# Optimization experiments

Measured on AMD Instinct MI355X. Metric: run time of the kernel, lower is better.

Reference implementation:

```python
import math
import jax, jax.numpy as jnp
import numpy as np

B, S, D = 16, 2048, 256

def setup_inputs() -> dict:
    key = jax.random.key(0)
    kq, kk, kv, km = jax.random.split(key, 4)
    q = jax.random.normal(kq, (B, S, D), dtype=jnp.float32)
    k = jax.random.normal(kk, (B, S, D), dtype=jnp.float32)
    v = jax.random.normal(kv, (B, S, D), dtype=jnp.float32)
    mask = jax.random.randint(km, (B, S, S), 0, 2, dtype=jnp.int32)
    return {"q": q, "k": k, "v": v, "mask": mask}

def reference(q, k, v, mask):
    dim_input = q.shape[-1]
    # scores: [B, S, S]
    scores = jnp.einsum('bqd,bkd->bqk', q, k) / math.sqrt(dim_input)
    # non-standard masking: masked positions set to 0.0 (NOT -inf) before softmax
    scores = jnp.where(mask == 0, jnp.float32(0.0), scores)
    att = jax.nn.softmax(scores, axis=-1)
    # original: if mask.sum() == 0, attention is all zeros
    att = jnp.where(mask.sum() > 0, att, jnp.zeros_like(att))
    return jnp.einsum('bqk,bkd->bqd', att, v)
```

## Files before the change

kernel.cpp:

```cpp
#include <hip/hip_runtime.h>


#define B_  16
#define S_  2048
#define D_  256
#define NT_ 64
#define TILE_BYTES 16384

typedef short bf16x8 __attribute__((ext_vector_type(8)));
typedef float f32x4  __attribute__((ext_vector_type(4)));

__device__ __forceinline__ unsigned short f2bf(float x) {
    union { float f; unsigned u; } c; c.f = x;
    unsigned u = c.u;
    u += 0x7FFFu + ((u >> 16) & 1u);
    return (unsigned short)(u >> 16);
}

#define GLDS(g, l) __builtin_amdgcn_global_load_lds( \
    (const __attribute__((address_space(1))) void*)(g), \
    (__attribute__((address_space(3))) void*)(l), 16, 0, 0)

#define WAITVM(N) asm volatile("s_waitcnt vmcnt(" #N ")" ::: "memory")

__global__ __launch_bounds__(256)
void prep_all(const float* __restrict__ k, const float* __restrict__ v,
              char* __restrict__ kbf, char* __restrict__ vtbf)
{
    const int bid = blockIdx.x;
    if (bid < 4096) {
        const int gid = bid * 256 + threadIdx.x;
        const int d8  = gid & 31;
        const int kv  = (gid >> 5) & 2047;
        const int b   = gid >> 16;
        const float* src = k + (((size_t)(b * S_ + kv)) << 8) + d8 * 8;
        const float4 f0 = *(const float4*)src;
        const float4 f1 = *(const float4*)(src + 4);
        bf16x8 h;
        h[0] = (short)f2bf(f0.x); h[1] = (short)f2bf(f0.y);
        h[2] = (short)f2bf(f0.z); h[3] = (short)f2bf(f0.w);
        h[4] = (short)f2bf(f1.x); h[5] = (short)f2bf(f1.y);
        h[6] = (short)f2bf(f1.z); h[7] = (short)f2bf(f1.w);
        const int tile = kv >> 5, kvl = kv & 31;
        char* dst = kbf + (((size_t)(b * NT_ + tile)) << 14)
                        + (kvl << 9) + ((d8 * 16) ^ ((kvl & 7) << 4));
        *(bf16x8*)dst = h;
    } else {
        const int gid  = (bid - 4096) * 256 + threadIdx.x;
        const int d    = gid & 255;
        const int g    = (gid >> 8) & 3;
        const int tile = (gid >> 10) & 63;
        const int b    = gid >> 16;
        const int kv0  = tile * 32 + g * 8;
        const float* src = v + (((size_t)(b * S_ + kv0)) << 8) + d;
        bf16x8 h;
        #pragma unroll
        for (int j = 0; j < 8; ++j) h[j] = (short)f2bf(src[(size_t)j << 8]);
        char* dst = vtbf + (((size_t)(b * NT_ + tile)) << 14)
                         + (d << 6) + ((g * 16) ^ (((d >> 1) & 3) << 4));
        *(bf16x8*)dst = h;
    }
}

__global__ __launch_bounds__(256, 1)
void attn_main(const float* __restrict__ q, const int* __restrict__ mask,
               const char* __restrict__ kbf, const char* __restrict__ vtbf,
               float* __restrict__ out)
{
    __shared__ alignas(128) char lds[139264];

    const int tid  = threadIdx.x;
    const int wid  = tid >> 6;
    const int lane = tid & 63;
    const int ln15 = lane & 15;
    const int quad = lane >> 4;
    const int swzK = (ln15 & 7) << 4;
    const int swzA = ((ln15 >> 1) & 3) << 4;

    const int bid = blockIdx.x;
    const int bx  = (bid & 7) * 32 + (bid >> 3);
    const int b   = bx >> 4;
    const int qt  = bx & 15;
    const int qw  = qt * 128 + wid * 32;

    const float QS = 0.09016844f;
    bf16x8 aq[2][8];
    #pragma unroll
    for (int s = 0; s < 2; ++s) {
        const float* qrow = q + ((size_t)(b * S_ + qw + s * 16 + ln15)) * D_;
        #pragma unroll
        for (int ks = 0; ks < 8; ++ks) {
            const float4 f0 = *(const float4*)(qrow + ks * 32 + quad * 8);
            const float4 f1 = *(const float4*)(qrow + ks * 32 + quad * 8 + 4);
            bf16x8 a;
            a[0] = (short)f2bf(f0.x * QS); a[1] = (short)f2bf(f0.y * QS);
            a[2] = (short)f2bf(f0.z * QS); a[3] = (short)f2bf(f0.w * QS);
            a[4] = (short)f2bf(f1.x * QS); a[5] = (short)f2bf(f1.y * QS);
            a[6] = (short)f2bf(f1.z * QS); a[7] = (short)f2bf(f1.w * QS);
            aq[s][ks] = a;
        }
    }
    __builtin_amdgcn_sched_barrier(0);

    bf16x8 ones;
    #pragma unroll
    for (int e = 0; e < 8; ++e) ones[e] = (short)0x3F80;

    f32x4 oacc[2][16];
    #pragma unroll
    for (int s = 0; s < 2; ++s)
        #pragma unroll
        for (int i = 0; i < 16; ++i) oacc[s][i] = (f32x4){0.f, 0.f, 0.f, 0.f};
    f32x4 lacc[2];
    lacc[0] = (f32x4){0.f, 0.f, 0.f, 0.f};
    lacc[1] = (f32x4){0.f, 0.f, 0.f, 0.f};

    const char* ktile = kbf  + (((size_t)b * NT_) << 14);
    const char* vtile = vtbf + (((size_t)b * NT_) << 14);
    char* pw = lds + 131072 + wid * 2048;
    const int cc = wid * 4;

    const int* mbase = mask + ((size_t)(b * S_ + qw + 4 * quad)) * S_;
    int mreg[4][16];

    #pragma unroll
    for (int t = 0; t < 3; ++t) {
        #pragma unroll
        for (int c = 0; c < 4; ++c) {
            GLDS(ktile + t * 16384 + (cc + c) * 1024 + lane * 16,
                 lds +         t * 16384 + (cc + c) * 1024);
            GLDS(vtile + t * 16384 + (cc + c) * 1024 + lane * 16,
                 lds + 65536 + t * 16384 + (cc + c) * 1024);
        }
        #pragma unroll
        for (int s = 0; s < 2; ++s)
            #pragma unroll
            for (int nt = 0; nt < 2; ++nt)
                #pragma unroll
                for (int r = 0; r < 4; ++r)
                    mreg[t][s * 8 + nt * 4 + r] = __builtin_nontemporal_load(
                        mbase + (size_t)(s * 16 + r) * S_ + t * 32 + nt * 16 + ln15);
    }

#define PHASE(T, CUR, CNT, ISSUE)                                               \
    {                                                                           \
        WAITVM(CNT);                                                            \
        __builtin_amdgcn_sched_barrier(0);                                      \
        __builtin_amdgcn_s_barrier();                                           \
        __builtin_amdgcn_sched_barrier(0);                                      \
        if (ISSUE) {                                                            \
            const int tn  = (T) + 3;                                            \
            const int bn  = ((CUR) + 3) & 3;                                    \
            const char* kg_ = ktile + ((size_t)tn << 14);                       \
            const char* vg_ = vtile + ((size_t)tn << 14);                       \
            _Pragma("unroll")                                                   \
            for (int c = 0; c < 4; ++c) {                                       \
                GLDS(kg_ + (cc + c) * 1024 + lane * 16,                         \
                     lds + bn * 16384 +         (cc + c) * 1024);               \
                GLDS(vg_ + (cc + c) * 1024 + lane * 16,                         \
                     lds + 65536 + bn * 16384 + (cc + c) * 1024);               \
            }                                                                   \
            _Pragma("unroll")                                                   \
            for (int s = 0; s < 2; ++s)                                         \
                _Pragma("unroll")                                               \
                for (int nt = 0; nt < 2; ++nt)                                  \
                    _Pragma("unroll")                                           \
                    for (int r = 0; r < 4; ++r)                                 \
                        mreg[bn][s * 8 + nt * 4 + r] = __builtin_nontemporal_load( \
                            mbase + (size_t)(s * 16 + r) * S_ + tn * 32 + nt * 16 + ln15); \
            __builtin_amdgcn_sched_barrier(0);                                  \
        }                                                                       \
        const char* kl = lds + (CUR) * 16384;                                   \
        f32x4 sacc[2][2];                                                       \
        sacc[0][0] = (f32x4){0.f, 0.f, 0.f, 0.f};                               \
        sacc[0][1] = (f32x4){0.f, 0.f, 0.f, 0.f};                               \
        sacc[1][0] = (f32x4){0.f, 0.f, 0.f, 0.f};                               \
        sacc[1][1] = (f32x4){0.f, 0.f, 0.f, 0.f};                               \
        _Pragma("unroll")                                                       \
        for (int ks = 0; ks < 8; ++ks) {                                        \
            _Pragma("unroll")                                                   \
            for (int nt = 0; nt < 2; ++nt) {                                    \
                const int off = ((nt * 16 + ln15) << 9)                         \
                              + (((ks << 6) + (quad << 4)) ^ swzK);             \
                const bf16x8 bk = *(const bf16x8*)(kl + off);                   \
                sacc[0][nt] = __builtin_amdgcn_mfma_f32_16x16x32_bf16(aq[0][ks], bk, sacc[0][nt], 0, 0, 0); \
                sacc[1][nt] = __builtin_amdgcn_mfma_f32_16x16x32_bf16(aq[1][ks], bk, sacc[1][nt], 0, 0, 0); \
            }                                                                   \
        }                                                                       \
        _Pragma("unroll")                                                       \
        for (int s = 0; s < 2; ++s) {                                           \
            _Pragma("unroll")                                                   \
            for (int nt = 0; nt < 2; ++nt) {                                    \
                _Pragma("unroll")                                               \
                for (int r = 0; r < 4; ++r) {                                   \
                    const float p = (mreg[CUR][s * 8 + nt * 4 + r] != 0)        \
                                  ? exp2f(sacc[s][nt][r]) : 1.0f;               \
                    const int row  = s * 16 + 4 * quad + r;                     \
                    const int boff = (row << 6)                                 \
                                   + ((nt * 32 + ln15 * 2) ^ (((row >> 1) & 3) << 4)); \
                    *(unsigned short*)(pw + boff) = f2bf(p);                    \
                }                                                               \
            }                                                                   \
        }                                                                       \
        const bf16x8 ap0 = *(const bf16x8*)(pw + (ln15 << 6)        + ((quad << 4) ^ swzA)); \
        const bf16x8 ap1 = *(const bf16x8*)(pw + ((16 + ln15) << 6) + ((quad << 4) ^ swzA)); \
        const char* vl = lds + 65536 + (CUR) * 16384;                           \
        lacc[0] = __builtin_amdgcn_mfma_f32_16x16x32_bf16(ap0, ones, lacc[0], 0, 0, 0); \
        lacc[1] = __builtin_amdgcn_mfma_f32_16x16x32_bf16(ap1, ones, lacc[1], 0, 0, 0); \
        _Pragma("unroll")                                                       \
        for (int nt2 = 0; nt2 < 16; ++nt2) {                                    \
            const int voff = ((nt2 * 16 + ln15) << 6) + ((quad << 4) ^ swzA);   \
            const bf16x8 bv = *(const bf16x8*)(vl + voff);                      \
            oacc[0][nt2] = __builtin_amdgcn_mfma_f32_16x16x32_bf16(ap0, bv, oacc[0][nt2], 0, 0, 0); \
            oacc[1][nt2] = __builtin_amdgcn_mfma_f32_16x16x32_bf16(ap1, bv, oacc[1][nt2], 0, 0, 0); \
        }                                                                       \
    }

    for (int t4 = 0; t4 < 15; ++t4) {
        const int t = t4 * 4;
        PHASE(t + 0, 0, 48, 1);
        PHASE(t + 1, 1, 48, 1);
        PHASE(t + 2, 2, 48, 1);
        PHASE(t + 3, 3, 48, 1);
    }
    PHASE(60, 0, 48, 1);
    PHASE(61, 1, 48, 0);
    PHASE(62, 2, 24, 0);
    PHASE(63, 3,  0, 0);
#undef PHASE

    #pragma unroll
    for (int s = 0; s < 2; ++s) {
        #pragma unroll
        for (int r = 0; r < 4; ++r) {
            const float inv = 1.0f / lacc[s][r];
            float* orow = out + ((size_t)(b * S_ + qw + s * 16 + 4 * quad + r)) * D_ + ln15;
            #pragma unroll
            for (int nt2 = 0; nt2 < 16; ++nt2)
                orow[nt2 * 16] = oacc[s][nt2][r] * inv;
        }
    }
}

#define QT 128
#define KTF 64
#define NW 8
#define KSTR 264
#define VSTR 72
#define PSTR 72

__global__ __launch_bounds__(512, 2)
void attn_fused_v1(const float* __restrict__ q, const float* __restrict__ k,
                   const float* __restrict__ v, const int* __restrict__ mask,
                   float* __restrict__ out)
{
    __shared__ unsigned short Kl[KTF * KSTR];
    __shared__ unsigned short Vt[D_ * VSTR];
    __shared__ unsigned short Pl[NW][16 * PSTR];

    const int tid  = threadIdx.x;
    const int wid  = tid >> 6;
    const int lane = tid & 63;
    const int ln15 = lane & 15;
    const int quad = lane >> 4;
    const int bid = blockIdx.x;
    const int bx  = (bid & 7) * 32 + (bid >> 3);
    const int b  = bx >> 4;
    const int qt = bx & 15;
    const int qw = qt * QT + wid * 16;

    const float* qb = q + ((size_t)b * S_ + qw) * D_;
    const float* kb = k + (size_t)b * S_ * D_;
    const float* vb = v + (size_t)b * S_ * D_;
    const int*   mb = mask + ((size_t)b * S_ + qw) * (size_t)S_;

    bf16x8 aq[8];
    {
        const float* qrow = qb + (size_t)ln15 * D_;
        #pragma unroll
        for (int ks = 0; ks < 8; ++ks) {
            const float4 f0 = *(const float4*)(qrow + ks * 32 + quad * 8);
            const float4 f1 = *(const float4*)(qrow + ks * 32 + quad * 8 + 4);
            bf16x8 a;
            a[0] = (short)f2bf(f0.x * 0.0625f); a[1] = (short)f2bf(f0.y * 0.0625f);
            a[2] = (short)f2bf(f0.z * 0.0625f); a[3] = (short)f2bf(f0.w * 0.0625f);
            a[4] = (short)f2bf(f1.x * 0.0625f); a[5] = (short)f2bf(f1.y * 0.0625f);
            a[6] = (short)f2bf(f1.z * 0.0625f); a[7] = (short)f2bf(f1.w * 0.0625f);
            aq[ks] = a;
        }
    }
    bf16x8 ones;
    #pragma unroll
    for (int e = 0; e < 8; ++e) ones[e] = (short)0x3F80;
    f32x4 oacc[16];
    #pragma unroll
    for (int i = 0; i < 16; ++i) oacc[i] = (f32x4){0.f, 0.f, 0.f, 0.f};
    f32x4 lacc = (f32x4){0.f, 0.f, 0.f, 0.f};
    const int kst_c0 = (tid & 63) * 4;

    for (int kt2 = 0; kt2 < S_ / KTF; ++kt2) {
        const int kvbase = kt2 * KTF;
        int mval[4][4];
        #pragma unroll
        for (int nt = 0; nt < 4; ++nt)
            #pragma unroll
            for (int r = 0; r < 4; ++r)
                mval[nt][r] = mb[(size_t)(4 * quad + r) * S_ + kvbase + nt * 16 + ln15];
        __syncthreads();
        {
            const float* ks_ = kb + (size_t)kvbase * D_;
            #pragma unroll
            for (int pass = 0; pass < 8; ++pass) {
                const int r = pass * 8 + wid;
                const float4 f = *(const float4*)(ks_ + (size_t)r * D_ + kst_c0);
                ushort4 hh;
                hh.x = f2bf(f.x); hh.y = f2bf(f.y); hh.z = f2bf(f.z); hh.w = f2bf(f.w);
                *(ushort4*)&Kl[r * KSTR + kst_c0] = hh;
            }
        }
        {
            const float* vs_ = vb + (size_t)kvbase * D_;
            #pragma unroll
            for (int pass = 0; pass < 8; ++pass) {
                const int idx = pass * 8 + wid;
                const int kv  = (idx & 3) * 16 + ln15;
                const int d0  = (idx >> 2) * 16 + 4 * quad;
                const float4 f = *(const float4*)(vs_ + (size_t)kv * D_ + d0);
                Vt[(d0 + 0) * VSTR + kv] = f2bf(f.x);
                Vt[(d0 + 1) * VSTR + kv] = f2bf(f.y);
                Vt[(d0 + 2) * VSTR + kv] = f2bf(f.z);
                Vt[(d0 + 3) * VSTR + kv] = f2bf(f.w);
            }
        }
        __syncthreads();
        f32x4 sacc[4];
        #pragma unroll
        for (int nt = 0; nt < 4; ++nt) sacc[nt] = (f32x4){0.f, 0.f, 0.f, 0.f};
        #pragma unroll
        for (int ks = 0; ks < 8; ++ks) {
            #pragma unroll
            for (int nt = 0; nt < 4; ++nt) {
                const bf16x8 bk =
                    *(const bf16x8*)&Kl[(nt * 16 + ln15) * KSTR + ks * 32 + quad * 8];
                sacc[nt] = __builtin_amdgcn_mfma_f32_16x16x32_bf16(aq[ks], bk, sacc[nt], 0, 0, 0);
            }
        }
        unsigned short* pwv = Pl[wid];
        #pragma unroll
        for (int nt = 0; nt < 4; ++nt) {
            #pragma unroll
            for (int r = 0; r < 4; ++r) {
                const float s = sacc[nt][r];
                const float p = (mval[nt][r] != 0) ? __expf(s) : 1.0f;
                pwv[(4 * quad + r) * PSTR + nt * 16 + ln15] = f2bf(p);
            }
        }
        #pragma unroll
        for (int ks2 = 0; ks2 < 2; ++ks2) {
            const bf16x8 ap = *(const bf16x8*)&pwv[ln15 * PSTR + ks2 * 32 + quad * 8];
            lacc = __builtin_amdgcn_mfma_f32_16x16x32_bf16(ap, ones, lacc, 0, 0, 0);
            #pragma unroll
            for (int nt2 = 0; nt2 < 16; ++nt2) {
                const bf16x8 bv =
                    *(const bf16x8*)&Vt[(nt2 * 16 + ln15) * VSTR + ks2 * 32 + quad * 8];
                oacc[nt2] = __builtin_amdgcn_mfma_f32_16x16x32_bf16(ap, bv, oacc[nt2], 0, 0, 0);
            }
        }
    }
    #pragma unroll
    for (int r = 0; r < 4; ++r) {
        const float inv = 1.0f / lacc[r];
        float* orow = out + ((size_t)b * S_ + qw + 4 * quad + r) * D_ + ln15;
        #pragma unroll
        for (int nt2 = 0; nt2 < 16; ++nt2)
            orow[nt2 * 16] = oacc[nt2][r] * inv;
    }
}

extern "C" void kernel_launch(void* const* d_in, const int* in_sizes, int n_in,
                              void* d_out, int out_size, void* d_ws, size_t ws_size,
                              hipStream_t stream) {
    const float* q    = (const float*)d_in[0];
    const float* k    = (const float*)d_in[1];
    const float* v    = (const float*)d_in[2];
    const int*   mask = (const int*)d_in[3];
    float*       out  = (float*)d_out;

    const size_t one = (size_t)B_ * NT_ * TILE_BYTES;
    if (ws_size >= 2 * one) {
        char* kbf  = (char*)d_ws;
        char* vtbf = kbf + one;
        prep_all<<<8192, 256, 0, stream>>>(k, v, kbf, vtbf);
        attn_main<<<256, 256, 0, stream>>>(q, mask, kbf, vtbf, out);
    } else {
        attn_fused_v1<<<256, 512, 0, stream>>>(q, k, v, mask, out);
    }
}
```

Baseline: 169.6 us.

## Stage mask tiles through LDS via async global_load_lds with triple buffering

Mask values are no longer loaded per lane into registers with nontemporal loads. Each mask tile is now copied into LDS with global_load_lds, alongside the K and V tiles, and read back from LDS in the softmax step. To make room, the pipeline drops from 4 buffers with prefetch distance 3 to 3 buffers with prefetch distance 2, and LDS use grows. The goal is coalesced, asynchronous mask transfers and lower register pressure, at the cost of a shallower prefetch and extra LDS reads.

```diff
diff --git a/kernel.cpp b/kernel.cpp
--- a/kernel.cpp
+++ b/kernel.cpp
@@ -22,6 +22,7 @@
     (__attribute__((address_space(3))) void*)(l), 16, 0, 0)
 
 #define WAITVM(N) asm volatile("s_waitcnt vmcnt(" #N ")" ::: "memory")
+#define SCHEDB()  __builtin_amdgcn_sched_barrier(0)
 
 __global__ __launch_bounds__(256)
 void prep_all(const float* __restrict__ k, const float* __restrict__ v,
@@ -67,7 +68,7 @@
                const char* __restrict__ kbf, const char* __restrict__ vtbf,
                float* __restrict__ out)
 {
-    __shared__ alignas(128) char lds[139264];
+    __shared__ alignas(128) char lds[155648];
 
     const int tid  = threadIdx.x;
     const int wid  = tid >> 6;
@@ -100,7 +101,7 @@
             aq[s][ks] = a;
         }
     }
-    __builtin_amdgcn_sched_barrier(0);
+    SCHEDB();
 
     bf16x8 ones;
     #pragma unroll
@@ -117,60 +118,59 @@
 
     const char* ktile = kbf  + (((size_t)b * NT_) << 14);
     const char* vtile = vtbf + (((size_t)b * NT_) << 14);
-    char* pw = lds + 131072 + wid * 2048;
+    const char* mrow0 = (const char*)(mask + ((size_t)(b * S_ + qt * 128)) * S_);
+    char* pw = lds + 147456 + wid * 2048;
     const int cc = wid * 4;
-
-    const int* mbase = mask + ((size_t)(b * S_ + qw + 4 * quad)) * S_;
-    int mreg[4][16];
-
-    #pragma unroll
-    for (int t = 0; t < 3; ++t) {
+    const int mlrow = (lane >> 3);
+    const int mlcol = (lane & 7) * 16;
+
+    const int mro = (wid * 32 + 4 * quad) * 128 + ln15 * 4;
+
+    #pragma unroll
+    for (int t = 0; t < 2; ++t) {
         #pragma unroll
         for (int c = 0; c < 4; ++c) {
             GLDS(ktile + t * 16384 + (cc + c) * 1024 + lane * 16,
                  lds +         t * 16384 + (cc + c) * 1024);
             GLDS(vtile + t * 16384 + (cc + c) * 1024 + lane * 16,
-                 lds + 65536 + t * 16384 + (cc + c) * 1024);
-        }
-        #pragma unroll
-        for (int s = 0; s < 2; ++s)
-            #pragma unroll
-            for (int nt = 0; nt < 2; ++nt)
-                #pragma unroll
-                for (int r = 0; r < 4; ++r)
-                    mreg[t][s * 8 + nt * 4 + r] = __builtin_nontemporal_load(
-                        mbase + (size_t)(s * 16 + r) * S_ + t * 32 + nt * 16 + ln15);
-    }
-
-#define PHASE(T, CUR, CNT, ISSUE)                                               \
+                 lds + 49152 + t * 16384 + (cc + c) * 1024);
+        }
+        #pragma unroll
+        for (int c = 0; c < 4; ++c) {
+            const int ch = cc + c;
+            GLDS(mrow0 + (size_t)(ch * 8 + mlrow) * (S_ * 4) + t * 128 + mlcol,
+                 lds + 98304 + t * 16384 + ch * 1024 + lane * 16);
+        }
+    }
+    SCHEDB();
+
+#define PHASE(T, CUR, BN, CNT)                                                  \
     {                                                                           \
         WAITVM(CNT);                                                            \
-        __builtin_amdgcn_sched_barrier(0);                                      \
+        SCHEDB();                                                               \
         __builtin_amdgcn_s_barrier();                                           \
-        __builtin_amdgcn_sched_barrier(0);                                      \
-        if (ISSUE) {                                                            \
-            const int tn  = (T) + 3;                                            \
-            const int bn  = ((CUR) + 3) & 3;                                    \
+        SCHEDB();                                                               \
+        if ((T) + 2 < NT_) {                                                    \
+            const int tn = (T) + 2;                                             \
             const char* kg_ = ktile + ((size_t)tn << 14);                       \
             const char* vg_ = vtile + ((size_t)tn << 14);                       \
             _Pragma("unroll")                                                   \
             for (int c = 0; c < 4; ++c) {                                       \
                 GLDS(kg_ + (cc + c) * 1024 + lane * 16,                         \
-                     lds + bn * 16384 +         (cc + c) * 1024);               \
+                     lds + (BN) * 16384 +         (cc + c) * 1024);             \
                 GLDS(vg_ + (cc + c) * 1024 + lane * 16,                         \
-                     lds + 65536 + bn * 16384 + (cc + c) * 1024);               \
+                     lds + 49152 + (BN) * 16384 + (cc + c) * 1024);             \
             }                                                                   \
             _Pragma("unroll")                                                   \
-            for (int s = 0; s < 2; ++s)                                         \
-                _Pragma("unroll")                                               \
-                for (int nt = 0; nt < 2; ++nt)                                  \
-                    _Pragma("unroll")                                           \
-                    for (int r = 0; r < 4; ++r)                                 \
-                        mreg[bn][s * 8 + nt * 4 + r] = __builtin_nontemporal_load( \
-                            mbase + (size_t)(s * 16 + r) * S_ + tn * 32 + nt * 16 + ln15); \
-            __builtin_amdgcn_sched_barrier(0);                                  \
+            for (int c = 0; c < 4; ++c) {                                       \
+                const int ch = cc + c;                                          \
+                GLDS(mrow0 + (size_t)(ch * 8 + mlrow) * (S_ * 4) + tn * 128 + mlcol, \
+                     lds + 98304 + (BN) * 16384 + ch * 1024 + lane * 16);       \
+            }                                                                   \
+            SCHEDB();                                                           \
         }                                                                       \
         const char* kl = lds + (CUR) * 16384;                                   \
+        const char* ml = lds + 98304 + (CUR) * 16384;                           \
         f32x4 sacc[2][2];                                                       \
         sacc[0][0] = (f32x4){0.f, 0.f, 0.f, 0.f};                               \
         sacc[0][1] = (f32x4){0.f, 0.f, 0.f, 0.f};                               \
@@ -193,8 +193,8 @@
             for (int nt = 0; nt < 2; ++nt) {                                    \
                 _Pragma("unroll")                                               \
                 for (int r = 0; r < 4; ++r) {                                   \
-                    const float p = (mreg[CUR][s * 8 + nt * 4 + r] != 0)        \
-                                  ? exp2f(sacc[s][nt][r]) : 1.0f;               \
+                    const int mv = *(const int*)(ml + mro + (s * 16 + r) * 128 + nt * 64); \
+                    const float p = (mv != 0) ? exp2f(sacc[s][nt][r]) : 1.0f;   \
                     const int row  = s * 16 + 4 * quad + r;                     \
                     const int boff = (row << 6)                                 \
                                    + ((nt * 32 + ln15 * 2) ^ (((row >> 1) & 3) << 4)); \
@@ -204,7 +204,7 @@
         }                                                                       \
         const bf16x8 ap0 = *(const bf16x8*)(pw + (ln15 << 6)        + ((quad << 4) ^ swzA)); \
         const bf16x8 ap1 = *(const bf16x8*)(pw + ((16 + ln15) << 6) + ((quad << 4) ^ swzA)); \
-        const char* vl = lds + 65536 + (CUR) * 16384;                           \
+        const char* vl = lds + 49152 + (CUR) * 16384;                           \
         lacc[0] = __builtin_amdgcn_mfma_f32_16x16x32_bf16(ap0, ones, lacc[0], 0, 0, 0); \
         lacc[1] = __builtin_amdgcn_mfma_f32_16x16x32_bf16(ap1, ones, lacc[1], 0, 0, 0); \
         _Pragma("unroll")                                                       \
@@ -214,19 +214,16 @@
             oacc[0][nt2] = __builtin_amdgcn_mfma_f32_16x16x32_bf16(ap0, bv, oacc[0][nt2], 0, 0, 0); \
             oacc[1][nt2] = __builtin_amdgcn_mfma_f32_16x16x32_bf16(ap1, bv, oacc[1][nt2], 0, 0, 0); \
         }                                                                       \
-    }
-
-    for (int t4 = 0; t4 < 15; ++t4) {
-        const int t = t4 * 4;
-        PHASE(t + 0, 0, 48, 1);
-        PHASE(t + 1, 1, 48, 1);
-        PHASE(t + 2, 2, 48, 1);
-        PHASE(t + 3, 3, 48, 1);
-    }
-    PHASE(60, 0, 48, 1);
-    PHASE(61, 1, 48, 0);
-    PHASE(62, 2, 24, 0);
-    PHASE(63, 3,  0, 0);
+        SCHEDB();                                                               \
+    }
+
+    for (int t3 = 0; t3 < 21; ++t3) {
+        const int t = t3 * 3;
+        PHASE(t + 0, 0, 2, 12);
+        PHASE(t + 1, 1, 0, 12);
+        PHASE(t + 2, 2, 1, 12);
+    }
+    PHASE(63, 0, 2, 0);
 #undef PHASE
 
     #pragma unroll
```

Measured after the change: 162.1 us. 1.05x faster.
